# Kernel tuning notes

Hardware: AMD Instinct MI355X
Metric: run time of the kernel (lower is better)

## Reference

```python
import jax, jax.numpy as jnp
import numpy as np

NEG_INF = -9e15  # matches torch's -9000000000000000.0 mask value


def setup_inputs() -> dict:
    key = jax.random.key(0)
    k1, k2, k3, k4 = jax.random.split(key, 4)
    B, F_in, T, N, F_out = 8, 64, 12, 512, 64
    inp = {
        "input": jax.random.normal(k1, (B, F_in, T, N), dtype=jnp.float32),
        "adj": jax.random.randint(k2, (B, T, N, N), 0, 2, dtype=jnp.int32),
        "W": jax.random.normal(k3, (F_in, F_out), dtype=jnp.float32),
        "a": jax.random.normal(k4, (2 * F_out, 1), dtype=jnp.float32),
    }
    return inp


def reference(input, adj, W, a):
    # input: [B, F_in, T, N], adj: [B, T, N, N]
    F_out = W.shape[1]
    x = jnp.transpose(input, (0, 2, 3, 1))          # [B, T, N, F_in]
    Wh = jnp.einsum('btnf,fo->btno', x, W)          # [B, T, N, F_out]
    # score decomposition: e[i,j] = leakyrelu(a1.Wh_i + a2.Wh_j)
    a1 = a[:F_out, 0]
    a2 = a[F_out:, 0]
    f1 = Wh @ a1                                    # [B, T, N]
    f2 = Wh @ a2                                    # [B, T, N]
    e = jax.nn.leaky_relu(f1[..., :, None] + f2[..., None, :], 0.2)
    e = jnp.where(adj > 0, e, NEG_INF)
    attn = jax.nn.softmax(e, axis=-1)               # [B, T, N, N]
    h = jnp.einsum('btij,btjo->btio', attn, Wh)     # [B, T, N, F_out]
    return jax.nn.elu(h)                            # concat=True -> elu
```

## Files before the change

kernel.cpp:

```cpp
#include <hip/hip_runtime.h>
#include <hip/hip_bf16.h>

typedef float fx4 __attribute__((ext_vector_type(4)));
typedef short i16x8 __attribute__((ext_vector_type(8)));
typedef unsigned short u16;

#define NEG_INF_F (-9.0e15f)

__device__ inline u16 f2bf(float v){
  __hip_bfloat16 h = __float2bfloat16(v);
  return *reinterpret_cast<u16*>(&h);
}
__device__ inline unsigned pk2(float lo, float hi){
  return (unsigned)f2bf(lo) | ((unsigned)f2bf(hi) << 16);
}

__global__ __launch_bounds__(256) void gat_prep(
    const float* __restrict__ input,
    const float* __restrict__ W,
    const float* __restrict__ Avec,
    u16*   __restrict__ whB,
    float* __restrict__ f1w,
    float* __restrict__ f2w)
{
  __shared__ float Wl[64*64];
  __shared__ float Al[128];
  __shared__ u16   Rp[16384];
  const int tid = threadIdx.x;
  const int bt  = blockIdx.y;
  const int b   = bt / 12, t = bt % 12;
  const int xb  = blockIdx.x;
  const int n   = xb * 256 + tid;

  {
    const fx4* src = (const fx4*)W;
    fx4* dst = (fx4*)Wl;
    #pragma unroll
    for (int i = 0; i < 4; ++i) dst[tid + 256*i] = src[tid + 256*i];
    if (tid < 32) ((fx4*)Al)[tid] = ((const fx4*)Avec)[tid];
  }
  __syncthreads();

  const float* xp = input + ((size_t)b*64*12 + t) * 512 + n;

  fx4 acc[16];
  #pragma unroll
  for (int i = 0; i < 16; ++i) acc[i] = (fx4){0.f,0.f,0.f,0.f};

  #pragma unroll 8
  for (int f = 0; f < 64; ++f) {
    float xv = xp[(size_t)f * 6144];
    const fx4* wr = (const fx4*)(Wl + f*64);
    #pragma unroll
    for (int o4 = 0; o4 < 16; ++o4) acc[o4] += xv * wr[o4];
  }

  float s1 = 0.f, s2 = 0.f;
  #pragma unroll
  for (int o4 = 0; o4 < 16; ++o4) {
    fx4 v  = acc[o4];
    fx4 w1 = ((const fx4*)Al)[o4];
    fx4 w2 = ((const fx4*)Al)[o4 + 16];
    s1 += v[0]*w1[0] + v[1]*w1[1] + v[2]*w1[2] + v[3]*w1[3];
    s2 += v[0]*w2[0] + v[1]*w2[1] + v[2]*w2[2] + v[3]*w2[3];
  }
  f1w[bt*512 + n] = s1;
  f2w[bt*512 + n] = s2;

  const int ktl  = (n >> 5) & 7;
  const int q    = (n >> 3) & 3;
  const int e    = n & 7;
  const int rowb = ktl*2048 + q*128 + e;
  #pragma unroll
  for (int o4 = 0; o4 < 16; ++o4) {
    #pragma unroll
    for (int c = 0; c < 4; ++c) {
      const int o = o4*4 + c;
      Rp[rowb + (o >> 4)*512 + (o & 15)*8] = f2bf(acc[o4][c]);
    }
  }
  __syncthreads();

  uint4* dst = (uint4*)(whB + ((size_t)bt*16 + xb*8) * 2048);
  const uint4* src = (const uint4*)Rp;
  #pragma unroll
  for (int i = 0; i < 8; ++i) dst[tid + 256*i] = src[tid + 256*i];
}

__global__ __launch_bounds__(256, 4) void gat_attn(
    const int*   __restrict__ adj,
    const u16*   __restrict__ whB,
    const float* __restrict__ f1w,
    const float* __restrict__ f2w,
    float*       __restrict__ out)
{
  __shared__ float f1l[16];
  __shared__ float wmaxl[4];
  __shared__ float sums[16];
  __shared__ unsigned char masknib[2048];
  __shared__ uint2 lutl[16];
  __shared__ u16   attnl[16*512];

  const int tid = threadIdx.x;
  const int l   = tid & 63;
  const int w   = tid >> 6;
  const int bt  = blockIdx.y;
  const int it  = blockIdx.x;

  const uint4* adjblk = (const uint4*)(adj + ((size_t)bt*512 + it*16)*512);
  uint4 av[8];
  #pragma unroll
  for (int i = 0; i < 8; ++i) av[i] = adjblk[tid + 256*i];

  const float* f2p = f2w + bt*512;
  const fx4 f20 = ((const fx4*)f2p)[l];
  const fx4 f21 = ((const fx4*)f2p)[64 + l];
  if (tid < 16) f1l[tid] = f1w[bt*512 + it*16 + tid];
  if (tid < 16) {
    const unsigned nb = tid;
    lutl[tid] = (uint2){ ((nb&1u)?0xFFFFu:0u) | ((nb&2u)?0xFFFF0000u:0u),
                         ((nb&4u)?0xFFFFu:0u) | ((nb&8u)?0xFFFF0000u:0u) };
  }
  float m2 = fmaxf(fmaxf(fmaxf(f20[0], f20[1]), fmaxf(f20[2], f20[3])),
                   fmaxf(fmaxf(f21[0], f21[1]), fmaxf(f21[2], f21[3])));
  #pragma unroll
  for (int off = 32; off >= 1; off >>= 1) m2 = fmaxf(m2, __shfl_xor(m2, off));
  if (l == 0) wmaxl[w] = m2;

  #pragma unroll
  for (int i = 0; i < 8; ++i) {
    unsigned nb = 0u;
    if ((int)av[i].x > 0) nb |= 1u;
    if ((int)av[i].y > 0) nb |= 2u;
    if ((int)av[i].z > 0) nb |= 4u;
    if ((int)av[i].w > 0) nb |= 8u;
    masknib[tid + 256*i] = (unsigned char)nb;
  }
  __syncthreads();
  const float F2max = fmaxf(fmaxf(wmaxl[0], wmaxl[1]), fmaxf(wmaxl[2], wmaxl[3]));

  fx4 v0, v1, vh0, vh1;
  #pragma unroll
  for (int c = 0; c < 4; ++c) {
    v0[c]  = __expf(f20[c] - F2max);
    v1[c]  = __expf(f21[c] - F2max);
    vh0[c] = __expf(0.2f*(f20[c] - F2max));
    vh1[c] = __expf(0.2f*(f21[c] - F2max));
  }
  const float thrBig = F2max - 80.f;
  const unsigned big_lo = (f20[0] > thrBig ? 1u : 0u) | (f20[1] > thrBig ? 2u : 0u)
                        | (f20[2] > thrBig ? 4u : 0u) | (f20[3] > thrBig ? 8u : 0u);
  const unsigned big_hi = (f21[0] > thrBig ? 1u : 0u) | (f21[1] > thrBig ? 2u : 0u)
                        | (f21[2] > thrBig ? 4u : 0u) | (f21[3] > thrBig ? 8u : 0u);

  const int R0 = w * 4;

  #pragma unroll
  for (int r = 0; r < 4; ++r) {
    const int rowR = R0 + r;
    const unsigned nib0 = masknib[rowR*128 + l];
    const unsigned nib1 = masknib[rowR*128 + 64 + l];
    const float f1v = f1l[rowR];

    unsigned w0, w1, w2, w3;
    const unsigned sb = (nib0 & big_lo) | (nib1 & big_hi);
    if (__builtin_expect(__any((int)sb), 1)) {
      const float tR = f1v + F2max;
      const float M  = fmaxf(tR, 0.2f*tR);
      const float u  = __expf(tR - M);
      const float uh = __expf(0.2f*tR - M);
      fx4 PA, PB;
      #pragma unroll
      for (int c = 0; c < 4; ++c) {
        PA[c] = fmaxf(u*v0[c], uh*vh0[c]);
        PB[c] = fmaxf(u*v1[c], uh*vh1[c]);
      }
      const uint2 mA = lutl[nib0];
      const uint2 mB = lutl[nib1];
      w0 = pk2(PA[0], PA[1]) & mA.x;
      w1 = pk2(PA[2], PA[3]) & mA.y;
      w2 = pk2(PB[0], PB[1]) & mB.x;
      w3 = pk2(PB[2], PB[3]) & mB.y;
    } else {
      float mx = NEG_INF_F;
      mx = fmaxf(mx, (nib0 & 1u) ? f20[0] : NEG_INF_F);
      mx = fmaxf(mx, (nib0 & 2u) ? f20[1] : NEG_INF_F);
      mx = fmaxf(mx, (nib0 & 4u) ? f20[2] : NEG_INF_F);
      mx = fmaxf(mx, (nib0 & 8u) ? f20[3] : NEG_INF_F);
      mx = fmaxf(mx, (nib1 & 1u) ? f21[0] : NEG_INF_F);
      mx = fmaxf(mx, (nib1 & 2u) ? f21[1] : NEG_INF_F);
      mx = fmaxf(mx, (nib1 & 4u) ? f21[2] : NEG_INF_F);
      mx = fmaxf(mx, (nib1 & 8u) ? f21[3] : NEG_INF_F);
      #pragma unroll
      for (int off = 32; off >= 1; off >>= 1) mx = fmaxf(mx, __shfl_xor(mx, off));
      const float tM = f1v + mx;
      const float Mc = fmaxf(tM, 0.2f*tM);
      const float Mf = (mx == NEG_INF_F) ? NEG_INF_F : Mc;
      float pv[8];
#define GAT_S(idx, bb_, ff) { float s = f1v + (ff); float lr = fmaxf(s, 0.2f*s); \
      float ee = (bb_) ? lr : NEG_INF_F; pv[idx] = __expf(ee - Mf); }
      GAT_S(0, nib0 & 1u, f20[0]) GAT_S(1, nib0 & 2u, f20[1])
      GAT_S(2, nib0 & 4u, f20[2]) GAT_S(3, nib0 & 8u, f20[3])
      GAT_S(4, nib1 & 1u, f21[0]) GAT_S(5, nib1 & 2u, f21[1])
      GAT_S(6, nib1 & 4u, f21[2]) GAT_S(7, nib1 & 8u, f21[3])
#undef GAT_S
      w0 = pk2(pv[0], pv[1]); w1 = pk2(pv[2], pv[3]);
      w2 = pk2(pv[4], pv[5]); w3 = pk2(pv[6], pv[7]);
    }

    const unsigned swz = (unsigned)((rowR & 7) << 4);
    char* base = (char*)attnl + rowR * 1024;
    *(uint2*)(base + (((unsigned)(      8*l)) ^ swz)) = (uint2){w0, w1};
    *(uint2*)(base + (((unsigned)(512 + 8*l)) ^ swz)) = (uint2){w2, w3};
  }
  __syncthreads();

  const int r = l & 15, q = l >> 4;
  const unsigned swzB = (unsigned)((r & 7) << 4);
  const char* aBase = (const char*)attnl + r * 1024;
  const u16*  wp    = whB + (size_t)bt*32768 + w*512 + l*8;
  i16x8 bones;
  #pragma unroll
  for (int e = 0; e < 8; ++e) bones[e] = (short)0x3F80;
  fx4 acc = {0,0,0,0}, accS = {0,0,0,0};

  #pragma unroll
  for (int kt = 0; kt < 16; ++kt) {
    i16x8 af = *(const i16x8*)(aBase + (((unsigned)(kt*64 + q*16)) ^ swzB));
    i16x8 bf = *(const i16x8*)(wp + kt*2048);
    acc = __builtin_amdgcn_mfma_f32_16x16x32_bf16(af, bf, acc, 0, 0, 0);
    if (w == 0)
      accS = __builtin_amdgcn_mfma_f32_16x16x32_bf16(af, bones, accS, 0, 0, 0);
  }
  if (w == 0 && r == 0) {
    #pragma unroll
    for (int rr = 0; rr < 4; ++rr) sums[q*4 + rr] = accS[rr];
  }
  __syncthreads();

  float* op = out + ((size_t)bt*512 + it*16) * 64;
  #pragma unroll
  for (int rr = 0; rr < 4; ++rr) {
    const float rs = 1.0f / sums[q*4 + rr];
    float v = acc[rr] * rs;
    v = v > 0.f ? v : expm1f(v);
    op[(q*4 + rr)*64 + w*16 + r] = v;
  }
}

extern "C" void kernel_launch(void* const* d_in, const int* in_sizes, int n_in,
                              void* d_out, int out_size, void* d_ws, size_t ws_size,
                              hipStream_t stream) {
  const float* input = (const float*)d_in[0];
  const int*   adj   = (const int*)  d_in[1];
  const float* W     = (const float*)d_in[2];
  const float* Avec  = (const float*)d_in[3];
  float* out = (float*)d_out;

  char* ws = (char*)d_ws;
  u16*   whB = (u16*)ws;
  float* f1w = (float*)(ws + 6291456);
  float* f2w = (float*)(ws + 6291456 + 196608);

  gat_prep<<<dim3(2, 96), 256, 0, stream>>>(input, W, Avec, whB, f1w, f2w);
  gat_attn<<<dim3(32, 96), 256, 0, stream>>>(adj, whB, f1w, f2w, out);
}
```

Before: 53.66 us.

## Give each wave its own 16 rows and build attention fragments in registers

Each block now covers 64 query rows, and each wave owns 16 rows across all 64 output columns with four accumulators plus a row-sum MFMA. Attention probabilities are built straight in registers from shared exp tables and a per-wave mask bitmap, which removes the shared-memory attention tile and the cross-wave sum exchange. The exact masked-max fallback now runs after the matmul, only when some row sum underflows, and redoes that wave's work. This cuts the grid from 3072 blocks to 768 and drops block-wide barriers. The cost is more registers per thread and less parallelism, since each block streams 128KB of adjacency with partly serialized loads.

```diff
diff --git a/kernel.cpp b/kernel.cpp
--- a/kernel.cpp
+++ b/kernel.cpp
@@ -94,157 +94,170 @@
     const float* __restrict__ f2w,
     float*       __restrict__ out)
 {
-  __shared__ float f1l[16];
+  __shared__ float ve[512], vhe[512], f2l[512];
+  __shared__ float f1l[64];
   __shared__ float wmaxl[4];
-  __shared__ float sums[16];
-  __shared__ unsigned char masknib[2048];
   __shared__ uint2 lutl[16];
-  __shared__ u16   attnl[16*512];
+  __shared__ unsigned maskws[4*272];
 
   const int tid = threadIdx.x;
   const int l   = tid & 63;
   const int w   = tid >> 6;
-  const int bt  = blockIdx.y;
-  const int it  = blockIdx.x;
-
-  const uint4* adjblk = (const uint4*)(adj + ((size_t)bt*512 + it*16)*512);
-  uint4 av[8];
-  #pragma unroll
-  for (int i = 0; i < 8; ++i) av[i] = adjblk[tid + 256*i];
-
-  const float* f2p = f2w + bt*512;
-  const fx4 f20 = ((const fx4*)f2p)[l];
-  const fx4 f21 = ((const fx4*)f2p)[64 + l];
-  if (tid < 16) f1l[tid] = f1w[bt*512 + it*16 + tid];
+  const int id  = blockIdx.x;
+  const int bt  = id >> 3;
+  const int g0  = (id & 7) * 64;
+  const int r   = l & 15, q = l >> 4;
+
+  const uint4* ablk = (const uint4*)(adj + ((size_t)bt*512 + g0 + w*16)*512);
+  uint4 A0[8], A1[8];
+  #pragma unroll
+  for (int i = 0; i < 8; ++i) A0[i] = ablk[l*8 + i];
+  #pragma unroll
+  for (int i = 0; i < 8; ++i) A1[i] = ablk[512 + l*8 + i];
+
+  float2 fv = ((const float2*)(f2w + bt*512))[tid];
+  ((float2*)f2l)[tid] = fv;
+  float m2 = fmaxf(fv.x, fv.y);
+  #pragma unroll
+  for (int off = 32; off >= 1; off >>= 1) m2 = fmaxf(m2, __shfl_xor(m2, off));
+  if (l == 0) wmaxl[w] = m2;
+  if (tid < 64) f1l[tid] = f1w[bt*512 + g0 + tid];
   if (tid < 16) {
     const unsigned nb = tid;
     lutl[tid] = (uint2){ ((nb&1u)?0xFFFFu:0u) | ((nb&2u)?0xFFFF0000u:0u),
                          ((nb&4u)?0xFFFFu:0u) | ((nb&8u)?0xFFFF0000u:0u) };
   }
-  float m2 = fmaxf(fmaxf(fmaxf(f20[0], f20[1]), fmaxf(f20[2], f20[3])),
-                   fmaxf(fmaxf(f21[0], f21[1]), fmaxf(f21[2], f21[3])));
-  #pragma unroll
-  for (int off = 32; off >= 1; off >>= 1) m2 = fmaxf(m2, __shfl_xor(m2, off));
-  if (l == 0) wmaxl[w] = m2;
-
-  #pragma unroll
-  for (int i = 0; i < 8; ++i) {
-    unsigned nb = 0u;
-    if ((int)av[i].x > 0) nb |= 1u;
-    if ((int)av[i].y > 0) nb |= 2u;
-    if ((int)av[i].z > 0) nb |= 4u;
-    if ((int)av[i].w > 0) nb |= 8u;
-    masknib[tid + 256*i] = (unsigned char)nb;
-  }
   __syncthreads();
   const float F2max = fmaxf(fmaxf(wmaxl[0], wmaxl[1]), fmaxf(wmaxl[2], wmaxl[3]));
-
-  fx4 v0, v1, vh0, vh1;
-  #pragma unroll
-  for (int c = 0; c < 4; ++c) {
-    v0[c]  = __expf(f20[c] - F2max);
-    v1[c]  = __expf(f21[c] - F2max);
-    vh0[c] = __expf(0.2f*(f20[c] - F2max));
-    vh1[c] = __expf(0.2f*(f21[c] - F2max));
-  }
-  const float thrBig = F2max - 80.f;
-  const unsigned big_lo = (f20[0] > thrBig ? 1u : 0u) | (f20[1] > thrBig ? 2u : 0u)
-                        | (f20[2] > thrBig ? 4u : 0u) | (f20[3] > thrBig ? 8u : 0u);
-  const unsigned big_hi = (f21[0] > thrBig ? 1u : 0u) | (f21[1] > thrBig ? 2u : 0u)
-                        | (f21[2] > thrBig ? 4u : 0u) | (f21[3] > thrBig ? 8u : 0u);
-
-  const int R0 = w * 4;
-
-  #pragma unroll
-  for (int r = 0; r < 4; ++r) {
-    const int rowR = R0 + r;
-    const unsigned nib0 = masknib[rowR*128 + l];
-    const unsigned nib1 = masknib[rowR*128 + 64 + l];
-    const float f1v = f1l[rowR];
-
-    unsigned w0, w1, w2, w3;
-    const unsigned sb = (nib0 & big_lo) | (nib1 & big_hi);
-    if (__builtin_expect(__any((int)sb), 1)) {
-      const float tR = f1v + F2max;
-      const float M  = fmaxf(tR, 0.2f*tR);
-      const float u  = __expf(tR - M);
-      const float uh = __expf(0.2f*tR - M);
-      fx4 PA, PB;
-      #pragma unroll
-      for (int c = 0; c < 4; ++c) {
-        PA[c] = fmaxf(u*v0[c], uh*vh0[c]);
-        PB[c] = fmaxf(u*v1[c], uh*vh1[c]);
-      }
-      const uint2 mA = lutl[nib0];
-      const uint2 mB = lutl[nib1];
-      w0 = pk2(PA[0], PA[1]) & mA.x;
-      w1 = pk2(PA[2], PA[3]) & mA.y;
-      w2 = pk2(PB[0], PB[1]) & mB.x;
-      w3 = pk2(PB[2], PB[3]) & mB.y;
-    } else {
-      float mx = NEG_INF_F;
-      mx = fmaxf(mx, (nib0 & 1u) ? f20[0] : NEG_INF_F);
-      mx = fmaxf(mx, (nib0 & 2u) ? f20[1] : NEG_INF_F);
-      mx = fmaxf(mx, (nib0 & 4u) ? f20[2] : NEG_INF_F);
-      mx = fmaxf(mx, (nib0 & 8u) ? f20[3] : NEG_INF_F);
-      mx = fmaxf(mx, (nib1 & 1u) ? f21[0] : NEG_INF_F);
-      mx = fmaxf(mx, (nib1 & 2u) ? f21[1] : NEG_INF_F);
-      mx = fmaxf(mx, (nib1 & 4u) ? f21[2] : NEG_INF_F);
-      mx = fmaxf(mx, (nib1 & 8u) ? f21[3] : NEG_INF_F);
-      #pragma unroll
-      for (int off = 32; off >= 1; off >>= 1) mx = fmaxf(mx, __shfl_xor(mx, off));
-      const float tM = f1v + mx;
-      const float Mc = fmaxf(tM, 0.2f*tM);
-      const float Mf = (mx == NEG_INF_F) ? NEG_INF_F : Mc;
+  ((float2*)ve)[tid]  = (float2){ __expf(fv.x - F2max),        __expf(fv.y - F2max) };
+  ((float2*)vhe)[tid] = (float2){ __expf(0.2f*(fv.x - F2max)), __expf(0.2f*(fv.y - F2max)) };
+  __syncthreads();
+
+  unsigned* mw = maskws + w*272;
+#define GAT_CONV(SRC, T) { unsigned wd = 0u; \
+  _Pragma("unroll") for (int i = 0; i < 8; ++i) { \
+    if ((int)SRC[i].x > 0) wd |= 1u << (4*i); \
+    if ((int)SRC[i].y > 0) wd |= 2u << (4*i); \
+    if ((int)SRC[i].z > 0) wd |= 4u << (4*i); \
+    if ((int)SRC[i].w > 0) wd |= 8u << (4*i); } \
+  mw[(l & 15)*17 + (T)*4 + (l >> 4)] = wd; }
+  GAT_CONV(A0, 0)
+  #pragma unroll
+  for (int i = 0; i < 8; ++i) A0[i] = ablk[1024 + l*8 + i];
+  GAT_CONV(A1, 1)
+  #pragma unroll
+  for (int i = 0; i < 8; ++i) A1[i] = ablk[1536 + l*8 + i];
+  GAT_CONV(A0, 2)
+  GAT_CONV(A1, 3)
+#undef GAT_CONV
+
+  const float f1v = f1l[w*16 + r];
+  const float tR  = f1v + F2max;
+  const float M   = fmaxf(tR, 0.2f*tR);
+  const float u   = __expf(tR - M);
+  const float uh  = __expf(0.2f*tR - M);
+  const u16* wb   = whB + (size_t)bt*32768 + l*8;
+  i16x8 bones;
+  #pragma unroll
+  for (int e = 0; e < 8; ++e) bones[e] = (short)0x3F80;
+  fx4 acc0 = {0,0,0,0}, acc1 = {0,0,0,0}, acc2 = {0,0,0,0}, acc3 = {0,0,0,0};
+  fx4 accS = {0,0,0,0};
+
+  #pragma unroll
+  for (int kt = 0; kt < 16; ++kt) {
+    const unsigned mword = mw[kt*17 + r];
+    const unsigned mb    = (mword >> (8*q)) & 0xFFu;
+    const fx4 a0 = ((const fx4*)ve)[kt*8 + 2*q];
+    const fx4 a1 = ((const fx4*)ve)[kt*8 + 2*q + 1];
+    const fx4 h0 = ((const fx4*)vhe)[kt*8 + 2*q];
+    const fx4 h1 = ((const fx4*)vhe)[kt*8 + 2*q + 1];
+    const uint2 mA = lutl[mb & 15u];
+    const uint2 mB = lutl[mb >> 4];
+    uint4 pw;
+    pw.x = pk2(fmaxf(u*a0[0], uh*h0[0]), fmaxf(u*a0[1], uh*h0[1])) & mA.x;
+    pw.y = pk2(fmaxf(u*a0[2], uh*h0[2]), fmaxf(u*a0[3], uh*h0[3])) & mA.y;
+    pw.z = pk2(fmaxf(u*a1[0], uh*h1[0]), fmaxf(u*a1[1], uh*h1[1])) & mB.x;
+    pw.w = pk2(fmaxf(u*a1[2], uh*h1[2]), fmaxf(u*a1[3], uh*h1[3])) & mB.y;
+    const i16x8 paf = *(const i16x8*)&pw;
+    const u16* bp = wb + kt*2048;
+    const i16x8 b0 = *(const i16x8*)(bp);
+    const i16x8 b1 = *(const i16x8*)(bp + 512);
+    const i16x8 b2 = *(const i16x8*)(bp + 1024);
+    const i16x8 b3 = *(const i16x8*)(bp + 1536);
+    acc0 = __builtin_amdgcn_mfma_f32_16x16x32_bf16(paf, b0, acc0, 0, 0, 0);
+    acc1 = __builtin_amdgcn_mfma_f32_16x16x32_bf16(paf, b1, acc1, 0, 0, 0);
+    acc2 = __builtin_amdgcn_mfma_f32_16x16x32_bf16(paf, b2, acc2, 0, 0, 0);
+    acc3 = __builtin_amdgcn_mfma_f32_16x16x32_bf16(paf, b3, acc3, 0, 0, 0);
+    accS = __builtin_amdgcn_mfma_f32_16x16x32_bf16(paf, bones, accS, 0, 0, 0);
+  }
+
+  const bool bad = (accS[0] < 1e-30f) || (accS[1] < 1e-30f) ||
+                   (accS[2] < 1e-30f) || (accS[3] < 1e-30f);
+  if (__any((int)bad)) {
+    float mx = NEG_INF_F;
+    #pragma unroll
+    for (int kt = 0; kt < 16; ++kt) {
+      const unsigned mb = (mw[kt*17 + r] >> (8*q)) & 0xFFu;
+      const fx4 g0v = ((const fx4*)f2l)[kt*8 + 2*q];
+      const fx4 g1v = ((const fx4*)f2l)[kt*8 + 2*q + 1];
+      mx = fmaxf(mx, (mb &   1u) ? g0v[0] : NEG_INF_F);
+      mx = fmaxf(mx, (mb &   2u) ? g0v[1] : NEG_INF_F);
+      mx = fmaxf(mx, (mb &   4u) ? g0v[2] : NEG_INF_F);
+      mx = fmaxf(mx, (mb &   8u) ? g0v[3] : NEG_INF_F);
+      mx = fmaxf(mx, (mb &  16u) ? g1v[0] : NEG_INF_F);
+      mx = fmaxf(mx, (mb &  32u) ? g1v[1] : NEG_INF_F);
+      mx = fmaxf(mx, (mb &  64u) ? g1v[2] : NEG_INF_F);
+      mx = fmaxf(mx, (mb & 128u) ? g1v[3] : NEG_INF_F);
+    }
+    mx = fmaxf(mx, __shfl_xor(mx, 16));
+    mx = fmaxf(mx, __shfl_xor(mx, 32));
+    const float tM = f1v + mx;
+    const float Mc = fmaxf(tM, 0.2f*tM);
+    const float Mf = (mx == NEG_INF_F) ? NEG_INF_F : Mc;
+    acc0 = acc1 = acc2 = acc3 = accS = (fx4){0,0,0,0};
+    #pragma unroll
+    for (int kt = 0; kt < 16; ++kt) {
+      const unsigned mb = (mw[kt*17 + r] >> (8*q)) & 0xFFu;
+      const fx4 g0v = ((const fx4*)f2l)[kt*8 + 2*q];
+      const fx4 g1v = ((const fx4*)f2l)[kt*8 + 2*q + 1];
       float pv[8];
 #define GAT_S(idx, bb_, ff) { float s = f1v + (ff); float lr = fmaxf(s, 0.2f*s); \
       float ee = (bb_) ? lr : NEG_INF_F; pv[idx] = __expf(ee - Mf); }
-      GAT_S(0, nib0 & 1u, f20[0]) GAT_S(1, nib0 & 2u, f20[1])
-      GAT_S(2, nib0 & 4u, f20[2]) GAT_S(3, nib0 & 8u, f20[3])
-      GAT_S(4, nib1 & 1u, f21[0]) GAT_S(5, nib1 & 2u, f21[1])
-      GAT_S(6, nib1 & 4u, f21[2]) GAT_S(7, nib1 & 8u, f21[3])
+      GAT_S(0, mb &   1u, g0v[0]) GAT_S(1, mb &   2u, g0v[1])
+      GAT_S(2, mb &   4u, g0v[2]) GAT_S(3, mb &   8u, g0v[3])
+      GAT_S(4, mb &  16u, g1v[0]) GAT_S(5, mb &  32u, g1v[1])
+      GAT_S(6, mb &  64u, g1v[2]) GAT_S(7, mb & 128u, g1v[3])
 #undef GAT_S
-      w0 = pk2(pv[0], pv[1]); w1 = pk2(pv[2], pv[3]);
-      w2 = pk2(pv[4], pv[5]); w3 = pk2(pv[6], pv[7]);
+      uint4 pw;
+      pw.x = pk2(pv[0], pv[1]); pw.y = pk2(pv[2], pv[3]);
+      pw.z = pk2(pv[4], pv[5]); pw.w = pk2(pv[6], pv[7]);
+      const i16x8 paf = *(const i16x8*)&pw;
+      const u16* bp = wb + kt*2048;
+      const i16x8 b0 = *(const i16x8*)(bp);
+      const i16x8 b1 = *(const i16x8*)(bp + 512);
+      const i16x8 b2 = *(const i16x8*)(bp + 1024);
+      const i16x8 b3 = *(const i16x8*)(bp + 1536);
+      acc0 = __builtin_amdgcn_mfma_f32_16x16x32_bf16(paf, b0, acc0, 0, 0, 0);
+      acc1 = __builtin_amdgcn_mfma_f32_16x16x32_bf16(paf, b1, acc1, 0, 0, 0);
+      acc2 = __builtin_amdgcn_mfma_f32_16x16x32_bf16(paf, b2, acc2, 0, 0, 0);
+      acc3 = __builtin_amdgcn_mfma_f32_16x16x32_bf16(paf, b3, acc3, 0, 0, 0);
+      accS = __builtin_amdgcn_mfma_f32_16x16x32_bf16(paf, bones, accS, 0, 0, 0);
     }
-
-    const unsigned swz = (unsigned)((rowR & 7) << 4);
-    char* base = (char*)attnl + rowR * 1024;
-    *(uint2*)(base + (((unsigned)(      8*l)) ^ swz)) = (uint2){w0, w1};
-    *(uint2*)(base + (((unsigned)(512 + 8*l)) ^ swz)) = (uint2){w2, w3};
-  }
-  __syncthreads();
-
-  const int r = l & 15, q = l >> 4;
-  const unsigned swzB = (unsigned)((r & 7) << 4);
-  const char* aBase = (const char*)attnl + r * 1024;
-  const u16*  wp    = whB + (size_t)bt*32768 + w*512 + l*8;
-  i16x8 bones;
-  #pragma unroll
-  for (int e = 0; e < 8; ++e) bones[e] = (short)0x3F80;
-  fx4 acc = {0,0,0,0}, accS = {0,0,0,0};
-
-  #pragma unroll
-  for (int kt = 0; kt < 16; ++kt) {
-    i16x8 af = *(const i16x8*)(aBase + (((unsigned)(kt*64 + q*16)) ^ swzB));
-    i16x8 bf = *(const i16x8*)(wp + kt*2048);
-    acc = __builtin_amdgcn_mfma_f32_16x16x32_bf16(af, bf, acc, 0, 0, 0);
-    if (w == 0)
-      accS = __builtin_amdgcn_mfma_f32_16x16x32_bf16(af, bones, accS, 0, 0, 0);
-  }
-  if (w == 0 && r == 0) {
-    #pragma unroll
-    for (int rr = 0; rr < 4; ++rr) sums[q*4 + rr] = accS[rr];
-  }
-  __syncthreads();
-
-  float* op = out + ((size_t)bt*512 + it*16) * 64;
+  }
+
+  float* op = out + ((size_t)bt*512 + g0 + w*16) * 64;
   #pragma unroll
   for (int rr = 0; rr < 4; ++rr) {
-    const float rs = 1.0f / sums[q*4 + rr];
-    float v = acc[rr] * rs;
-    v = v > 0.f ? v : expm1f(v);
-    op[(q*4 + rr)*64 + w*16 + r] = v;
+    const float rs = 1.0f / accS[rr];
+    float v0 = acc0[rr] * rs; v0 = v0 > 0.f ? v0 : expm1f(v0);
+    float v1 = acc1[rr] * rs; v1 = v1 > 0.f ? v1 : expm1f(v1);
+    float v2 = acc2[rr] * rs; v2 = v2 > 0.f ? v2 : expm1f(v2);
+    float v3 = acc3[rr] * rs; v3 = v3 > 0.f ? v3 : expm1f(v3);
+    float* o = op + (q*4 + rr)*64 + r;
+    o[ 0] = v0;
+    o[16] = v1;
+    o[32] = v2;
+    o[48] = v3;
   }
 }
 
@@ -263,5 +276,5 @@
   float* f2w = (float*)(ws + 6291456 + 196608);
 
   gat_prep<<<dim3(2, 96), 256, 0, stream>>>(input, W, Avec, whB, f1w, f2w);
-  gat_attn<<<dim3(32, 96), 256, 0, stream>>>(adj, whB, f1w, f2w, out);
-}
+  gat_attn<<<768, 256, 0, stream>>>(adj, whB, f1w, f2w, out);
+}
```

Result: slower. 117.6 us (+119.1%).
